# Optimization experiments

Measured on AMD Instinct MI355X. Metric: run time of the kernel, lower is better.

Reference implementation:

```python
import jax, jax.numpy as jnp
import numpy as np

VOCAB = 2048
CHORD_VOCAB = 60
SCALE_W = 0.1
REP_W = 0.05
CHORD_W = 0.2
WINDOW = 8  # repetition look-back window


def setup_inputs() -> dict:
    key = jax.random.key(0)
    ks = jax.random.split(key, 7)
    B, S = 4, 2048
    return {
        "logits": jax.random.normal(ks[0], (B, S, VOCAB), dtype=jnp.float32),
        "chord_logits": jax.random.normal(ks[1], (B, S, CHORD_VOCAB), dtype=jnp.float32),
        "scale_logits": jax.random.normal(ks[2], (B, S, 12), dtype=jnp.float32),
        "scale_targets": jax.random.uniform(ks[3], (B, S, 12), dtype=jnp.float32),
        "target_ids": jax.random.randint(ks[4], (B, S), 0, VOCAB, dtype=jnp.int64),
        "key_ids": jax.random.randint(ks[5], (B,), 0, 12, dtype=jnp.int64),
        "chord_targets": jax.random.randint(ks[6], (B, S), 0, CHORD_VOCAB, dtype=jnp.int64),
    }


def _ce_ignore(logits, targets, ignore_index=-100):
    # cross entropy with ignore_index, mean over valid tokens
    logp = jax.nn.log_softmax(logits, axis=-1)
    valid = (targets != ignore_index)
    safe = jnp.where(valid, targets, 0)
    nll = -jnp.take_along_axis(logp, safe[..., None], axis=-1)[..., 0]
    denom = jnp.maximum(valid.sum(), 1)
    return jnp.sum(nll * valid) / denom.astype(logits.dtype)


def _repetition_loss(target_ids, dtype):
    # input_ids = [0, target_ids[:, :-1]] (teacher-forced inputs)
    B, S = target_ids.shape
    input_ids = jnp.concatenate(
        [jnp.zeros((B, 1), dtype=target_ids.dtype), target_ids[:, :-1]], axis=1)
    # sliding-window histogram: counts[b,pos,v] = #{t in [max(0,pos-8), pos) : ids[b,t]==v}
    oh = jax.nn.one_hot(input_ids, VOCAB, dtype=dtype)          # [B,S,V]
    cs = jnp.cumsum(oh, axis=1)                                  # cs[p] = sum_{0..p}
    a = jnp.pad(cs, ((0, 0), (1, 0), (0, 0)))[:, :S]             # cs[pos-1]
    b = jnp.pad(cs, ((0, 0), (WINDOW + 1, 0), (0, 0)))[:, :S]    # cs[pos-9]
    counts = a - b                                               # zero at pos=0 automatically
    # penalty = -0.5*counts; rep_loss = -penalty.mean() = 0.5*mean(counts)
    return 0.5 * jnp.mean(counts)


def _bce_with_logits(x, z):
    # numerically stable mean BCE-with-logits
    return jnp.mean(jnp.maximum(x, 0) - x * z + jnp.log1p(jnp.exp(-jnp.abs(x))))


def reference(logits, chord_logits, scale_logits, scale_targets,
              target_ids, key_ids, chord_targets):
    main_loss = _ce_ignore(logits, target_ids)
    rep_loss = _repetition_loss(target_ids, logits.dtype)
    chord_loss = _ce_ignore(chord_logits, chord_targets, ignore_index=-(10**9))  # no ignores present
    scale_loss = _bce_with_logits(scale_logits, scale_targets)
    total = main_loss + REP_W * rep_loss + CHORD_W * chord_loss + SCALE_W * scale_loss
    return total
```

## Files before the change

kernel.cpp:

```cpp
#include <hip/hip_runtime.h>
#include <math.h>


#define VOCAB 2048
#define CHORDV 60

typedef float vf4 __attribute__((ext_vector_type(4)));

__device__ __forceinline__ float waveRedMax(float v) {
#pragma unroll
    for (int off = 32; off > 0; off >>= 1)
        v = fmaxf(v, __shfl_xor(v, off, 64));
    return v;
}

__device__ __forceinline__ float waveRedSum(float v) {
#pragma unroll
    for (int off = 32; off > 0; off >>= 1)
        v += __shfl_xor(v, off, 64);
    return v;
}

__device__ __forceinline__ float bce1(float x, float z) {
    return fmaxf(x, 0.0f) - x * z + __logf(1.0f + __expf(-fabsf(x)));
}

__global__ __launch_bounds__(256) void fused_leaf_kernel(
    const float* __restrict__ logits, const int* __restrict__ tgt,
    const float* __restrict__ chordL, const int* __restrict__ chordT,
    const float* __restrict__ sx, const float* __restrict__ sz,
    float2* __restrict__ mainNV, float2* __restrict__ chordNV,
    float* __restrict__ scaleP, int BS, int chordBlocks, int n4) {
    const int bid = blockIdx.x;
    const int tid = threadIdx.x;
    const int lane = tid & 63;
    const int wave = tid >> 6;

    __shared__ float red[4];
    __shared__ float xt_sh;
    __shared__ float2 csh[4];

    if (bid < BS) {
        const int row = bid;
        const int t = tgt[row];
        const float* p = logits + (size_t)row * VOCAB;

        vf4 a = __builtin_nontemporal_load(((const vf4*)p) + tid);
        vf4 b = __builtin_nontemporal_load(((const vf4*)p) + tid + 256);

        const bool valid = (t >= 0) && (t < VOCAB);
        if (valid) {
            const int owner = t >> 2;
            const int comp = t & 3;
            if (owner == tid) {
                xt_sh = a[comp];
            } else if (owner == tid + 256) {
                xt_sh = b[comp];
            }
        }

        float m = fmaxf(fmaxf(fmaxf(a[0], a[1]), fmaxf(a[2], a[3])),
                        fmaxf(fmaxf(b[0], b[1]), fmaxf(b[2], b[3])));
        float wm = waveRedMax(m);
        if (lane == 0) red[wave] = wm;
        __syncthreads();
        const float bm = fmaxf(fmaxf(red[0], red[1]), fmaxf(red[2], red[3]));
        __syncthreads();

        float s = __expf(a[0] - bm) + __expf(a[1] - bm) + __expf(a[2] - bm) + __expf(a[3] - bm)
                + __expf(b[0] - bm) + __expf(b[1] - bm) + __expf(b[2] - bm) + __expf(b[3] - bm);
        float ws_ = waveRedSum(s);
        if (lane == 0) red[wave] = ws_;
        __syncthreads();

        if (tid == 0) {
            const float bs = red[0] + red[1] + red[2] + red[3];
            float2 nv = make_float2(0.0f, 0.0f);
            if (valid) {
                nv.x = -(xt_sh - bm - __logf(bs));
                nv.y = 1.0f;
            }
            mainNV[row] = nv;
        }
    } else if (bid < BS + chordBlocks) {
        const int cb = bid - BS;
        const int row = cb * 4 + wave;
        float2 nv = make_float2(0.0f, 0.0f);
        if (row < BS) {
            const float* p = chordL + (size_t)row * CHORDV;
            const int t = chordT[row];
            float x = (lane < CHORDV) ? p[lane] : -INFINITY;
            float m = waveRedMax(x);
            float e = (lane < CHORDV) ? __expf(x - m) : 0.0f;
            float s = waveRedSum(e);
            if (t != -1000000000) {
                nv.x = -(p[t] - m - __logf(s));
                nv.y = 1.0f;
            }
        }
        if (lane == 0) csh[wave] = nv;
        __syncthreads();
        if (tid == 0) {
            chordNV[cb] = make_float2(csh[0].x + csh[1].x + csh[2].x + csh[3].x,
                                      csh[0].y + csh[1].y + csh[2].y + csh[3].y);
        }
    } else {
        const int sb = bid - BS - chordBlocks;
        const int i = sb * 256 + tid;
        float s = 0.0f;
        if (i < n4) {
            float4 xv = ((const float4*)sx)[i];
            float4 zv = ((const float4*)sz)[i];
            s = bce1(xv.x, zv.x) + bce1(xv.y, zv.y) + bce1(xv.z, zv.z) + bce1(xv.w, zv.w);
        }
        float wsum = waveRedSum(s);
        if (lane == 0) red[wave] = wsum;
        __syncthreads();
        if (tid == 0) scaleP[sb] = red[0] + red[1] + red[2] + red[3];
    }
}

__device__ __forceinline__ float blockSum1024(float v, float* red16) {
    const int lane = threadIdx.x & 63;
    const int wave = threadIdx.x >> 6;
    float w = waveRedSum(v);
    __syncthreads();
    if (lane == 0) red16[wave] = w;
    __syncthreads();
    float r = 0.0f;
#pragma unroll
    for (int k = 0; k < 16; ++k) r += red16[k];
    return r;
}

__global__ __launch_bounds__(1024) void finalize_kernel(
    const float2* __restrict__ mainNV, const float2* __restrict__ chordNV,
    const float* __restrict__ scaleP, int BS, int chordBlocks, int nScaleBlocks,
    int S, int scaleN, float* __restrict__ out) {
    const int tid = threadIdx.x;
    float sm = 0.f, svm = 0.f, sc = 0.f, svc = 0.f, ss = 0.f;

    const float4* m4 = (const float4*)mainNV;
    for (int i = tid; i < BS / 2; i += 1024) {
        float4 v = m4[i];
        sm += v.x + v.z;
        svm += v.y + v.w;
    }
    if ((BS & 1) && tid == 0) { float2 v = mainNV[BS - 1]; sm += v.x; svm += v.y; }

    const float4* c4 = (const float4*)chordNV;
    for (int i = tid; i < chordBlocks / 2; i += 1024) {
        float4 v = c4[i];
        sc += v.x + v.z;
        svc += v.y + v.w;
    }
    if ((chordBlocks & 1) && tid == 0) { float2 v = chordNV[chordBlocks - 1]; sc += v.x; svc += v.y; }

    for (int i = tid; i < nScaleBlocks; i += 1024) ss += scaleP[i];

    __shared__ float red16[16];
    sm  = blockSum1024(sm,  red16);
    svm = blockSum1024(svm, red16);
    sc  = blockSum1024(sc,  red16);
    svc = blockSum1024(svc, red16);
    ss  = blockSum1024(ss,  red16);

    if (tid == 0) {
        const float main_loss  = sm / fmaxf(svm, 1.0f);
        const float chord_loss = sc / fmaxf(svc, 1.0f);
        const float scale_loss = ss / (float)scaleN;
        double wsum = (S >= 8) ? (28.0 + 8.0 * (double)(S - 8))
                               : ((double)S * (double)(S - 1) * 0.5);
        const float rep_loss = (float)(0.5 * wsum / ((double)S * (double)VOCAB));
        out[0] = main_loss + 0.05f * rep_loss + 0.2f * chord_loss + 0.1f * scale_loss;
    }
}

extern "C" void kernel_launch(void* const* d_in, const int* in_sizes, int n_in,
                              void* d_out, int out_size, void* d_ws, size_t ws_size,
                              hipStream_t stream) {
    const float* logits        = (const float*)d_in[0];
    const float* chord_logits  = (const float*)d_in[1];
    const float* scale_logits  = (const float*)d_in[2];
    const float* scale_targets = (const float*)d_in[3];
    const int*   target_ids    = (const int*)d_in[4];
    const int*   chord_targets = (const int*)d_in[6];

    const int BS = in_sizes[4];
    const int B  = in_sizes[5];
    const int S  = BS / B;
    const int scaleN = in_sizes[2];
    const int n4 = scaleN / 4;
    const int nScaleBlocks = (n4 + 255) / 256;
    const int chordBlocks = (BS + 3) / 4;

    float2* mainNV  = (float2*)d_ws;
    float2* chordNV = mainNV + BS;
    float*  scaleP  = (float*)(chordNV + chordBlocks);

    const int totalBlocks = BS + chordBlocks + nScaleBlocks;
    fused_leaf_kernel<<<totalBlocks, 256, 0, stream>>>(
        logits, target_ids, chord_logits, chord_targets,
        scale_logits, scale_targets, mainNV, chordNV, scaleP,
        BS, chordBlocks, n4);
    finalize_kernel<<<1, 1024, 0, stream>>>(mainNV, chordNV, scaleP,
                                            BS, chordBlocks, nScaleBlocks,
                                            S, scaleN, (float*)d_out);
}
```

Measured before the change: 114.2 us.

## Map one vocab row per wavefront instead of per block for main CE

The main cross-entropy path now assigns one row to each 64-lane wavefront, with four rows per block. Max and sum reductions stay inside the wave, the target logit is fetched with a shuffle instead of through shared memory, and per-block partial sums are written out. This removes three block-wide barriers per row and cuts the block count by four, at the cost of 32 floats held in registers per lane. The chord path also reads its target logit with a shuffle instead of a second global load, and nontemporal loads are added for the chord and scale inputs.

```diff
diff --git a/kernel.cpp b/kernel.cpp
--- a/kernel.cpp
+++ b/kernel.cpp
@@ -30,87 +30,95 @@
     const float* __restrict__ chordL, const int* __restrict__ chordT,
     const float* __restrict__ sx, const float* __restrict__ sz,
     float2* __restrict__ mainNV, float2* __restrict__ chordNV,
-    float* __restrict__ scaleP, int BS, int chordBlocks, int n4) {
+    float* __restrict__ scaleP, int BS, int mainBlocks, int chordBlocks, int n4) {
     const int bid = blockIdx.x;
     const int tid = threadIdx.x;
     const int lane = tid & 63;
     const int wave = tid >> 6;
 
+    __shared__ float2 sh2[4];
     __shared__ float red[4];
-    __shared__ float xt_sh;
-    __shared__ float2 csh[4];
-
-    if (bid < BS) {
-        const int row = bid;
-        const int t = tgt[row];
-        const float* p = logits + (size_t)row * VOCAB;
-
-        vf4 a = __builtin_nontemporal_load(((const vf4*)p) + tid);
-        vf4 b = __builtin_nontemporal_load(((const vf4*)p) + tid + 256);
-
-        const bool valid = (t >= 0) && (t < VOCAB);
-        if (valid) {
-            const int owner = t >> 2;
-            const int comp = t & 3;
-            if (owner == tid) {
-                xt_sh = a[comp];
-            } else if (owner == tid + 256) {
-                xt_sh = b[comp];
+
+    if (bid < mainBlocks) {
+        const int row = bid * 4 + wave;
+        float2 nv = make_float2(0.0f, 0.0f);
+        if (row < BS) {
+            const int t = tgt[row];
+            const vf4* p4 = (const vf4*)(logits + (size_t)row * VOCAB);
+
+            vf4 v[8];
+#pragma unroll
+            for (int k = 0; k < 8; ++k)
+                v[k] = __builtin_nontemporal_load(p4 + lane + 64 * k);
+
+            float m = -INFINITY;
+#pragma unroll
+            for (int k = 0; k < 8; ++k)
+                m = fmaxf(m, fmaxf(fmaxf(v[k].x, v[k].y), fmaxf(v[k].z, v[k].w)));
+            m = waveRedMax(m);
+
+            float s = 0.0f;
+#pragma unroll
+            for (int k = 0; k < 8; ++k)
+                s += __expf(v[k].x - m) + __expf(v[k].y - m) +
+                     __expf(v[k].z - m) + __expf(v[k].w - m);
+            s = waveRedSum(s);
+
+            const bool valid = (t >= 0) && (t < VOCAB);
+            if (valid) {
+                const int vi = t >> 2;
+                const int owner = vi & 63;
+                const int chunk = vi >> 6;
+                const int comp = t & 3;
+                float cand = 0.0f;
+#pragma unroll
+                for (int k = 0; k < 8; ++k) {
+                    if (chunk == k) {
+                        const float lo = (comp & 1) ? v[k].y : v[k].x;
+                        const float hi = (comp & 1) ? v[k].w : v[k].z;
+                        cand = (comp & 2) ? hi : lo;
+                    }
+                }
+                const float xt = __shfl(cand, owner, 64);
+                nv.x = -(xt - m - __logf(s));
+                nv.y = 1.0f;
             }
         }
-
-        float m = fmaxf(fmaxf(fmaxf(a[0], a[1]), fmaxf(a[2], a[3])),
-                        fmaxf(fmaxf(b[0], b[1]), fmaxf(b[2], b[3])));
-        float wm = waveRedMax(m);
-        if (lane == 0) red[wave] = wm;
+        if (lane == 0) sh2[wave] = nv;
         __syncthreads();
-        const float bm = fmaxf(fmaxf(red[0], red[1]), fmaxf(red[2], red[3]));
-        __syncthreads();
-
-        float s = __expf(a[0] - bm) + __expf(a[1] - bm) + __expf(a[2] - bm) + __expf(a[3] - bm)
-                + __expf(b[0] - bm) + __expf(b[1] - bm) + __expf(b[2] - bm) + __expf(b[3] - bm);
-        float ws_ = waveRedSum(s);
-        if (lane == 0) red[wave] = ws_;
-        __syncthreads();
-
-        if (tid == 0) {
-            const float bs = red[0] + red[1] + red[2] + red[3];
-            float2 nv = make_float2(0.0f, 0.0f);
-            if (valid) {
-                nv.x = -(xt_sh - bm - __logf(bs));
-                nv.y = 1.0f;
-            }
-            mainNV[row] = nv;
-        }
-    } else if (bid < BS + chordBlocks) {
-        const int cb = bid - BS;
+        if (tid == 0)
+            mainNV[bid] = make_float2(sh2[0].x + sh2[1].x + sh2[2].x + sh2[3].x,
+                                      sh2[0].y + sh2[1].y + sh2[2].y + sh2[3].y);
+    } else if (bid < mainBlocks + chordBlocks) {
+        const int cb = bid - mainBlocks;
         const int row = cb * 4 + wave;
         float2 nv = make_float2(0.0f, 0.0f);
         if (row < BS) {
             const float* p = chordL + (size_t)row * CHORDV;
             const int t = chordT[row];
-            float x = (lane < CHORDV) ? p[lane] : -INFINITY;
+            float x = (lane < CHORDV) ? __builtin_nontemporal_load(p + lane) : -INFINITY;
             float m = waveRedMax(x);
             float e = (lane < CHORDV) ? __expf(x - m) : 0.0f;
             float s = waveRedSum(e);
             if (t != -1000000000) {
-                nv.x = -(p[t] - m - __logf(s));
+                const int tt = (t >= 0 && t < CHORDV) ? t : 0;
+                const float xt = __shfl(x, tt, 64);
+                nv.x = -(xt - m - __logf(s));
                 nv.y = 1.0f;
             }
         }
-        if (lane == 0) csh[wave] = nv;
+        if (lane == 0) sh2[wave] = nv;
         __syncthreads();
-        if (tid == 0) {
-            chordNV[cb] = make_float2(csh[0].x + csh[1].x + csh[2].x + csh[3].x,
-                                      csh[0].y + csh[1].y + csh[2].y + csh[3].y);
-        }
+        if (tid == 0)
+            chordNV[cb] = make_float2(sh2[0].x + sh2[1].x + sh2[2].x + sh2[3].x,
+                                      sh2[0].y + sh2[1].y + sh2[2].y + sh2[3].y);
     } else {
-        const int sb = bid - BS - chordBlocks;
+        const int sb = bid - mainBlocks - chordBlocks;
         const int i = sb * 256 + tid;
         float s = 0.0f;
         if (i < n4) {
-            float4 xv = ((const float4*)sx)[i];
-            float4 zv = ((const float4*)sz)[i];
+            vf4 xv = __builtin_nontemporal_load(((const vf4*)sx) + i);
+            vf4 zv = __builtin_nontemporal_load(((const vf4*)sz) + i);
             s = bce1(xv.x, zv.x) + bce1(xv.y, zv.y) + bce1(xv.z, zv.z) + bce1(xv.w, zv.w);
         }
         float wsum = waveRedSum(s);
@@ -135,18 +143,18 @@
 
 __global__ __launch_bounds__(1024) void finalize_kernel(
     const float2* __restrict__ mainNV, const float2* __restrict__ chordNV,
-    const float* __restrict__ scaleP, int BS, int chordBlocks, int nScaleBlocks,
+    const float* __restrict__ scaleP, int mainBlocks, int chordBlocks, int nScaleBlocks,
     int S, int scaleN, float* __restrict__ out) {
     const int tid = threadIdx.x;
     float sm = 0.f, svm = 0.f, sc = 0.f, svc = 0.f, ss = 0.f;
 
     const float4* m4 = (const float4*)mainNV;
-    for (int i = tid; i < BS / 2; i += 1024) {
+    for (int i = tid; i < mainBlocks / 2; i += 1024) {
         float4 v = m4[i];
         sm += v.x + v.z;
         svm += v.y + v.w;
     }
-    if ((BS & 1) && tid == 0) { float2 v = mainNV[BS - 1]; sm += v.x; svm += v.y; }
+    if ((mainBlocks & 1) && tid == 0) { float2 v = mainNV[mainBlocks - 1]; sm += v.x; svm += v.y; }
 
     const float4* c4 = (const float4*)chordNV;
     for (int i = tid; i < chordBlocks / 2; i += 1024) {
@@ -192,18 +200,19 @@
     const int scaleN = in_sizes[2];
     const int n4 = scaleN / 4;
     const int nScaleBlocks = (n4 + 255) / 256;
+    const int mainBlocks  = (BS + 3) / 4;
     const int chordBlocks = (BS + 3) / 4;
 
     float2* mainNV  = (float2*)d_ws;
-    float2* chordNV = mainNV + BS;
+    float2* chordNV = mainNV + mainBlocks;
     float*  scaleP  = (float*)(chordNV + chordBlocks);
 
-    const int totalBlocks = BS + chordBlocks + nScaleBlocks;
+    const int totalBlocks = mainBlocks + chordBlocks + nScaleBlocks;
     fused_leaf_kernel<<<totalBlocks, 256, 0, stream>>>(
         logits, target_ids, chord_logits, chord_targets,
         scale_logits, scale_targets, mainNV, chordNV, scaleP,
-        BS, chordBlocks, n4);
+        BS, mainBlocks, chordBlocks, n4);
     finalize_kernel<<<1, 1024, 0, stream>>>(mainNV, chordNV, scaleP,
-                                            BS, chordBlocks, nScaleBlocks,
+                                            mainBlocks, chordBlocks, nScaleBlocks,
                                             S, scaleN, (float*)d_out);
 }
```

After: 113.6 us. No clear change (-0.6%).
